# Kernel optimization log

Measured on AMD Instinct MI355X. Metric: run time of the kernel, lower is better.

## Reference

```python
import jax, jax.numpy as jnp
import numpy as np

N_HEADS = 16
LN_EPS = 1e-5


def setup_inputs() -> dict:
    key = jax.random.key(0)
    k_z, k_qkv, k_proj = jax.random.split(key, 3)
    b, n, dm = 4, 2048, 1024
    z = jax.random.normal(k_z, (b, n, dm), dtype=jnp.float32)
    gamma = jnp.ones((dm,), dtype=jnp.float32)
    beta = jnp.zeros((dm,), dtype=jnp.float32)
    # parameterize Linear weights as (in, out) so y = x @ w (same math as torch x @ W.T)
    w_qkv = jax.random.normal(k_qkv, (dm, 3 * dm), dtype=jnp.float32) * (1.0 / np.sqrt(dm))
    w_proj = jax.random.normal(k_proj, (dm, dm), dtype=jnp.float32) * (1.0 / np.sqrt(dm))
    b_proj = jnp.zeros((dm,), dtype=jnp.float32)
    return {"z": z, "gamma": gamma, "beta": beta, "w_qkv": w_qkv,
            "w_proj": w_proj, "b_proj": b_proj}


def reference(z, gamma, beta, w_qkv, w_proj, b_proj):
    b, n, dm = z.shape
    h = N_HEADS
    d = dm // h
    scaling = jnp.asarray(np.sqrt(dm / h), dtype=z.dtype)

    # LayerNorm over last dim
    mu = jnp.mean(z, axis=-1, keepdims=True)
    var = jnp.mean(jnp.square(z - mu), axis=-1, keepdims=True)
    zn = (z - mu) * jax.lax.rsqrt(var + LN_EPS) * gamma + beta

    qkv = zn @ w_qkv  # [b, n, 3*dm]
    # einops 'b n (h d qkv_n) -> qkv_n b h n d': qkv index is INNERMOST of packed dim
    qkv = qkv.reshape(b, n, h, d, 3)
    q = qkv[..., 0]  # [b, n, h, d]
    k = qkv[..., 1]
    v = qkv[..., 2]

    scores = jnp.einsum('bqhd,bkhd->bhqk', q, k) / scaling  # [b, h, n, n]
    att = jax.nn.softmax(scores, axis=-1)
    out = jnp.einsum('bhqk,bkhd->bqhd', att, v).reshape(b, n, dm)
    out = out @ w_proj + b_proj  # projection (drop_hidden=False); dropout is identity in eval
    return z + out
```

## Files before the change

kernel.cpp:

```cpp
#include <hip/hip_runtime.h>

typedef unsigned short ushort;
typedef unsigned int uint;

typedef __bf16 bf16x8 __attribute__((ext_vector_type(8)));
typedef float floatx4 __attribute__((ext_vector_type(4)));

constexpr int BATCH = 4;
constexpr int SEQ = 2048;
constexpr int DM = 1024;
constexpr int NH = 16;
constexpr int HD = 64;
constexpr int M = BATCH * SEQ;
constexpr int NQKV = 3 * DM;
constexpr float QSCALE = 0.18033688011112042f;

__device__ __forceinline__ ushort f2b(float f) {
    uint x; __builtin_memcpy(&x, &f, 4);
    x += 0x7fffu + ((x >> 16) & 1u);
    return (ushort)(x >> 16);
}

__device__ __forceinline__ void gload16(const ushort* g, ushort* l) {
    __builtin_amdgcn_global_load_lds(
        (const __attribute__((address_space(1))) void*)g,
        (__attribute__((address_space(3))) void*)l, 16, 0, 0);
}

__global__ __launch_bounds__(256) void prep_kernel(
    const float* __restrict__ w_qkv, ushort* __restrict__ wqT,
    const float* __restrict__ w_proj, ushort* __restrict__ wpT,
    const float* __restrict__ z, const float* __restrict__ gamma,
    const float* __restrict__ beta, ushort* __restrict__ zn) {
    __shared__ ushort tile[64][65];
    int id = blockIdx.x;
    int t = threadIdx.x;
    if (id < 1024) {
        int tx = t & 63, ty = t >> 6;
        if (id < 768) {
            int bx = id % 48, by = id / 48;
            int c0 = bx * 64, r0 = by * 64;
#pragma unroll
            for (int i = 0; i < 64; i += 4)
                tile[i + ty][tx] = f2b(w_qkv[(size_t)(r0 + i + ty) * NQKV + c0 + tx]);
            __syncthreads();
#pragma unroll
            for (int i = 0; i < 64; i += 4) {
                int c = c0 + i + ty;
                int cp = (c % 3) * DM + c / 3;
                wqT[(size_t)cp * DM + r0 + tx] = tile[tx][i + ty];
            }
        } else {
            int q = id - 768;
            int c0 = (q % 16) * 64, r0 = (q / 16) * 64;
#pragma unroll
            for (int i = 0; i < 64; i += 4)
                tile[i + ty][tx] = f2b(w_proj[(size_t)(r0 + i + ty) * DM + c0 + tx]);
            __syncthreads();
#pragma unroll
            for (int i = 0; i < 64; i += 4)
                wpT[(size_t)(c0 + i + ty) * DM + r0 + tx] = tile[tx][i + ty];
        }
        return;
    }
    int row = id - 1024;
    float4 v = reinterpret_cast<const float4*>(z + (size_t)row * DM)[t];
    float s = v.x + v.y + v.z + v.w;
    float sq = v.x * v.x + v.y * v.y + v.z * v.z + v.w * v.w;
#pragma unroll
    for (int off = 32; off >= 1; off >>= 1) {
        s  += __shfl_xor(s, off);
        sq += __shfl_xor(sq, off);
    }
    __shared__ float red[8];
    int wave = t >> 6;
    if ((t & 63) == 0) { red[wave] = s; red[wave + 4] = sq; }
    __syncthreads();
    s  = red[0] + red[1] + red[2] + red[3];
    sq = red[4] + red[5] + red[6] + red[7];
    float mean = s * (1.f / DM);
    float var  = sq * (1.f / DM) - mean * mean;
    float rstd = rsqrtf(var + 1e-5f);
    float4 g = reinterpret_cast<const float4*>(gamma)[t];
    float4 bt = reinterpret_cast<const float4*>(beta)[t];
    ushort4 o;
    o.x = f2b((v.x - mean) * rstd * g.x + bt.x);
    o.y = f2b((v.y - mean) * rstd * g.y + bt.y);
    o.z = f2b((v.z - mean) * rstd * g.z + bt.z);
    o.w = f2b((v.w - mean) * rstd * g.w + bt.w);
    reinterpret_cast<ushort4*>(zn + (size_t)row * DM)[t] = o;
}

__device__ __forceinline__ void gemm128_core(
    const ushort* __restrict__ A, const ushort* __restrict__ BT,
    int m0, int n0, int t, floatx4 (&acc)[4][4],
    ushort (*As)[64], ushort (*Bs)[64]) {
    int lane = t & 63, w = t >> 6;
    int l16 = lane & 15, quad = lane >> 4;
    int wm = (w >> 1) * 64, wn = (w & 1) * 64;
#pragma unroll
    for (int i = 0; i < 4; i++)
#pragma unroll
        for (int j = 0; j < 4; j++) acc[i][j] = (floatx4){0.f, 0.f, 0.f, 0.f};

    int srow8 = lane >> 3;
    int lseg = (lane & 7) ^ srow8;
    const ushort* gA[4]; const ushort* gB[4];
    ushort* lA[4]; ushort* lB[4];
#pragma unroll
    for (int c = 0; c < 4; c++) {
        int r = 32 * c + 8 * w + srow8;
        gA[c] = &A [(size_t)(m0 + r) * DM + lseg * 8];
        gB[c] = &BT[(size_t)(n0 + r) * DM + lseg * 8];
        lA[c] = &As[32 * c + 8 * w][0];
        lB[c] = &Bs[32 * c + 8 * w][0];
    }
    int sw = l16 & 7;

    for (int k0 = 0; k0 < DM; k0 += 64) {
#pragma unroll
        for (int c = 0; c < 4; c++) {
            gload16(gA[c] + k0, lA[c]);
            gload16(gB[c] + k0, lB[c]);
        }
        __syncthreads();
#pragma unroll
        for (int kk = 0; kk < 2; kk++) {
            bf16x8 af[4], bf[4];
#pragma unroll
            for (int i = 0; i < 4; i++)
                af[i] = *reinterpret_cast<const bf16x8*>(
                    &As[wm + i * 16 + l16][((kk * 4 + quad) ^ sw) << 3]);
#pragma unroll
            for (int j = 0; j < 4; j++)
                bf[j] = *reinterpret_cast<const bf16x8*>(
                    &Bs[wn + j * 16 + l16][((kk * 4 + quad) ^ sw) << 3]);
#pragma unroll
            for (int i = 0; i < 4; i++)
#pragma unroll
                for (int j = 0; j < 4; j++)
                    acc[i][j] = __builtin_amdgcn_mfma_f32_16x16x32_bf16(
                        af[i], bf[j], acc[i][j], 0, 0, 0);
        }
        __syncthreads();
    }
}

__global__ __launch_bounds__(256) void gemm_qkv(
    const ushort* __restrict__ A,
    const ushort* __restrict__ BT,
    ushort* __restrict__ Q, ushort* __restrict__ K, ushort* __restrict__ V) {
    __shared__ ushort smem[16384];
    ushort (*As)[64] = (ushort(*)[64])smem;
    ushort (*Bs)[64] = (ushort(*)[64])(smem + 8192);
    ushort* Cs = smem;
    int t = threadIdx.x;
    int id = blockIdx.x;
    int m0 = (id & 63) * 128, n0 = (id >> 6) * 128;
    floatx4 acc[4][4];
    gemm128_core(A, BT, m0, n0, t, acc, As, Bs);
    int lane = t & 63, w = t >> 6;
    int l16 = lane & 15, quad = lane >> 4;
    int wn = (w & 1) * 64;
    int which = n0 >> 10;
    int hd0 = n0 & 1023;
    float scale = (which == 0) ? QSCALE : 1.0f;
    int bb = m0 >> 11;
    int nb = m0 & 2047;
    ushort* dstQK = (which == 0) ? Q : K;

#pragma unroll
    for (int p = 0; p < 2; p++) {
        __syncthreads();
        if ((w >> 1) == p) {
            if (which < 2) {
#pragma unroll
                for (int i = 0; i < 4; i++)
#pragma unroll
                    for (int j = 0; j < 4; j++)
#pragma unroll
                        for (int r = 0; r < 4; r++)
                            Cs[(i * 16 + quad * 4 + r) * 136 + wn + j * 16 + l16] =
                                f2b(acc[i][j][r] * scale);
            } else {
#pragma unroll
                for (int i = 0; i < 4; i++)
#pragma unroll
                    for (int j = 0; j < 4; j++)
#pragma unroll
                        for (int r = 0; r < 4; r++)
                            Cs[(wn + j * 16 + l16) * 72 + i * 16 + quad * 4 + r] =
                                f2b(acc[i][j][r]);
            }
        }
        __syncthreads();
        if (which < 2) {
            int ch = (t & 15) * 8;
#pragma unroll
            for (int u = 0; u < 4; u++) {
                int lr = (t >> 4) + u * 16;
                int n = nb + p * 64 + lr;
                int hh = (hd0 + ch) >> 6, dd = ch & 63;
                *reinterpret_cast<uint4*>(
                    &dstQK[((size_t)((bb * NH + hh) * SEQ) + n) * HD + dd]) =
                    *reinterpret_cast<const uint4*>(&Cs[lr * 136 + ch]);
            }
        } else {
            int nch = (t & 7) * 8;
#pragma unroll
            for (int u = 0; u < 4; u++) {
                int dc = (t >> 3) + u * 32;
                int hh = (hd0 >> 6) + (dc >> 6), dd = dc & 63;
                int n = nb + p * 64 + nch;
                *reinterpret_cast<uint4*>(
                    &V[((size_t)((bb * NH + hh) * HD) + dd) * SEQ + n]) =
                    *reinterpret_cast<const uint4*>(&Cs[dc * 72 + nch]);
            }
        }
    }
}

__global__ __launch_bounds__(256) void gemm_proj(
    const ushort* __restrict__ A,
    const ushort* __restrict__ BT,
    const float* __restrict__ bias, const float* __restrict__ z,
    float* __restrict__ out) {
    __shared__ ushort As[128][64];
    __shared__ ushort Bs[128][64];
    int t = threadIdx.x;
    int id = blockIdx.x;
    int m0 = (id & 63) * 128, n0 = (id >> 6) * 128;
    floatx4 acc[4][4];
    gemm128_core(A, BT, m0, n0, t, acc, As, Bs);
    int lane = t & 63, w = t >> 6;
    int l16 = lane & 15, quad = lane >> 4;
    int wm = (w >> 1) * 64, wn = (w & 1) * 64;
#pragma unroll
    for (int j = 0; j < 4; j++) {
        int col = n0 + wn + j * 16 + l16;
        float bz = bias[col];
#pragma unroll
        for (int i = 0; i < 4; i++) {
#pragma unroll
            for (int r = 0; r < 4; r++) {
                int row = m0 + wm + i * 16 + quad * 4 + r;
                out[(size_t)row * DM + col] =
                    acc[i][j][r] + bz + z[(size_t)row * DM + col];
            }
        }
    }
}

__global__ __launch_bounds__(256) void attn_kernel(
    const ushort* __restrict__ Q, const ushort* __restrict__ K,
    const ushort* __restrict__ Vt, ushort* __restrict__ O) {
    __shared__ ushort QsPs[128 * 64];
    __shared__ ushort Ks[64 * 64];
    __shared__ ushort Vs[64 * 64];
    int t = threadIdx.x;
    int lane = t & 63, w = t >> 6;
    int l16 = lane & 15, quad = lane >> 4;
    int id = blockIdx.x;
    int qt = id >> 6, bh = id & 63;
    int bb = bh >> 4, h = bh & 15;
    int q0 = qt * 128;
    const ushort* Qg = Q  + (size_t)((bb * NH + h) * SEQ + q0) * HD;
    const ushort* Kg = K  + (size_t)((bb * NH + h) * SEQ) * HD;
    const ushort* Vg = Vt + (size_t)((bb * NH + h) * HD) * SEQ;

    int srow = lane >> 3;
    int lseg = (lane & 7) ^ srow;
    int r0 = 8 * w + srow;

    gload16(Qg + (size_t)r0 * HD + lseg * 8,         &QsPs[w * 512]);
    gload16(Qg + (size_t)(32 + r0) * HD + lseg * 8,  &QsPs[2048 + w * 512]);
    gload16(Qg + (size_t)(64 + r0) * HD + lseg * 8,  &QsPs[4096 + w * 512]);
    gload16(Qg + (size_t)(96 + r0) * HD + lseg * 8,  &QsPs[6144 + w * 512]);
    gload16(Kg + (size_t)r0 * HD + lseg * 8,         &Ks[w * 512]);
    gload16(Kg + (size_t)(32 + r0) * HD + lseg * 8,  &Ks[2048 + w * 512]);
    gload16(Vg + (size_t)r0 * SEQ + lseg * 8,        &Vs[w * 512]);
    gload16(Vg + (size_t)(32 + r0) * SEQ + lseg * 8, &Vs[2048 + w * 512]);
    __syncthreads();

    int swl = l16 & 7;
    bf16x8 aq[2][2];
    ushort* PsRow[2];
#pragma unroll
    for (int g = 0; g < 2; g++) {
        int row = 32 * w + 16 * g + l16;
        aq[g][0] = *reinterpret_cast<const bf16x8*>(&QsPs[row * 64 + ((quad ^ swl) << 3)]);
        aq[g][1] = *reinterpret_cast<const bf16x8*>(&QsPs[row * 64 + (((quad + 4) ^ swl) << 3)]);
        PsRow[g] = &QsPs[row * 64];
    }

    size_t koff1 = (size_t)r0 * HD + lseg * 8;
    size_t koff2 = (size_t)(32 + r0) * HD + lseg * 8;
    size_t voff1 = (size_t)r0 * SEQ + lseg * 8;
    size_t voff2 = (size_t)(32 + r0) * SEQ + lseg * 8;
    ushort* kw1 = &Ks[w * 512 + (lane & 63) * 8];
    ushort* kw2 = &Ks[2048 + w * 512 + (lane & 63) * 8];
    ushort* vw1 = &Vs[w * 512 + (lane & 63) * 8];
    ushort* vw2 = &Vs[2048 + w * 512 + (lane & 63) * 8];
    const ushort* Kp = Kg + (size_t)64 * HD;
    const ushort* Vp = Vg + 64;

    bf16x8 bones;
    {
        union { ushort u[8]; bf16x8 v; } cvt;
        ushort one = (l16 == 0) ? (ushort)0x3F80 : (ushort)0;
#pragma unroll
        for (int i = 0; i < 8; i++) cvt.u[i] = one;
        bones = cvt.v;
    }

    floatx4 Oacc[2][4], lacc[2];
#pragma unroll
    for (int g = 0; g < 2; g++) {
        lacc[g] = (floatx4){0.f, 0.f, 0.f, 0.f};
#pragma unroll
        for (int tt = 0; tt < 4; tt++) Oacc[g][tt] = (floatx4){0.f, 0.f, 0.f, 0.f};
    }

    constexpr int NT = SEQ / 64;
    for (int kt = 0; kt < NT; kt++) {
        uint4 kr1 = *reinterpret_cast<const uint4*>(Kp + koff1);
        uint4 kr2 = *reinterpret_cast<const uint4*>(Kp + koff2);
        uint4 vr1 = *reinterpret_cast<const uint4*>(Vp + voff1);
        uint4 vr2 = *reinterpret_cast<const uint4*>(Vp + voff2);
        Kp += (size_t)64 * HD;
        Vp += 64;

        floatx4 sacc[2][4];
#pragma unroll
        for (int nt = 0; nt < 4; nt++) {
            bf16x8 ak0 = *reinterpret_cast<const bf16x8*>(&Ks[(nt * 16 + l16) * 64 + ((quad ^ swl) << 3)]);
            bf16x8 ak1 = *reinterpret_cast<const bf16x8*>(&Ks[(nt * 16 + l16) * 64 + (((quad + 4) ^ swl) << 3)]);
#pragma unroll
            for (int g = 0; g < 2; g++) {
                floatx4 sv = (floatx4){0.f, 0.f, 0.f, 0.f};
                sv = __builtin_amdgcn_mfma_f32_16x16x32_bf16(ak0, aq[g][0], sv, 0, 0, 0);
                sv = __builtin_amdgcn_mfma_f32_16x16x32_bf16(ak1, aq[g][1], sv, 0, 0, 0);
                sacc[g][nt] = sv;
            }
        }
#pragma unroll
        for (int g = 0; g < 2; g++) {
#pragma unroll
            for (int nt = 0; nt < 4; nt++) {
                float p0 = __builtin_amdgcn_exp2f(sacc[g][nt][0]);
                float p1 = __builtin_amdgcn_exp2f(sacc[g][nt][1]);
                float p2 = __builtin_amdgcn_exp2f(sacc[g][nt][2]);
                float p3 = __builtin_amdgcn_exp2f(sacc[g][nt][3]);
                uint b0, b1, b2, b3;
                __builtin_memcpy(&b0, &p0, 4); __builtin_memcpy(&b1, &p1, 4);
                __builtin_memcpy(&b2, &p2, 4); __builtin_memcpy(&b3, &p3, 4);
                uint2 pk;
                pk.x = __builtin_amdgcn_perm(b1, b0, 0x07060302u);
                pk.y = __builtin_amdgcn_perm(b3, b2, 0x07060302u);
                int lseg2 = 2 * nt + (quad >> 1);
                *reinterpret_cast<uint2*>(&PsRow[g][((lseg2 ^ swl) << 3) + (quad & 1) * 4]) = pk;
            }
        }
#pragma unroll
        for (int ks = 0; ks < 2; ks++) {
            bf16x8 ap[2];
#pragma unroll
            for (int g = 0; g < 2; g++) {
                ap[g] = *reinterpret_cast<const bf16x8*>(
                    &PsRow[g][(((4 * ks + quad) ^ swl) << 3)]);
                lacc[g] = __builtin_amdgcn_mfma_f32_16x16x32_bf16(ap[g], bones, lacc[g], 0, 0, 0);
            }
#pragma unroll
            for (int tt = 0; tt < 4; tt++) {
                bf16x8 bv = *reinterpret_cast<const bf16x8*>(
                    &Vs[(tt * 16 + l16) * 64 + ((((ks * 4 + quad)) ^ swl) << 3)]);
#pragma unroll
                for (int g = 0; g < 2; g++)
                    Oacc[g][tt] = __builtin_amdgcn_mfma_f32_16x16x32_bf16(ap[g], bv, Oacc[g][tt], 0, 0, 0);
            }
        }
        __syncthreads();
        *reinterpret_cast<uint4*>(kw1) = kr1;
        *reinterpret_cast<uint4*>(kw2) = kr2;
        *reinterpret_cast<uint4*>(vw1) = vr1;
        *reinterpret_cast<uint4*>(vw2) = vr2;
        __syncthreads();
    }
    float lq[2][4];
#pragma unroll
    for (int g = 0; g < 2; g++)
#pragma unroll
        for (int j = 0; j < 4; j++) lq[g][j] = __shfl(lacc[g][j], quad << 4);

#pragma unroll
    for (int g = 0; g < 2; g++) {
#pragma unroll
        for (int tt = 0; tt < 4; tt++) {
#pragma unroll
            for (int j = 0; j < 4; j++) {
                int n = q0 + 32 * w + 16 * g + quad * 4 + j;
                int dcol = tt * 16 + l16;
                float val = Oacc[g][tt][j] / lq[g][j];
                O[(size_t)(bb * SEQ + n) * DM + h * HD + dcol] = f2b(val);
            }
        }
    }
}

extern "C" void kernel_launch(void* const* d_in, const int* in_sizes, int n_in,
                              void* d_out, int out_size, void* d_ws, size_t ws_size,
                              hipStream_t stream) {
    const float* z      = (const float*)d_in[0];
    const float* gamma  = (const float*)d_in[1];
    const float* beta   = (const float*)d_in[2];
    const float* w_qkv  = (const float*)d_in[3];
    const float* w_proj = (const float*)d_in[4];
    const float* b_proj = (const float*)d_in[5];
    float* out = (float*)d_out;

    char* ws = (char*)d_ws;
    const size_t SZ = (size_t)M * DM * sizeof(ushort);
    ushort* zn   = (ushort*)(ws);
    ushort* Qb   = (ushort*)(ws + SZ);
    ushort* Kb   = (ushort*)(ws + 2 * SZ);
    ushort* Vb   = (ushort*)(ws + 3 * SZ);
    ushort* wqT  = (ushort*)(ws + 4 * SZ);
    ushort* wpT  = (ushort*)(ws + 4 * SZ + (size_t)DM * NQKV * sizeof(ushort));
    ushort* Ob = zn;

    prep_kernel<<<1024 + M, 256, 0, stream>>>(w_qkv, wqT, w_proj, wpT,
                                              z, gamma, beta, zn);
    gemm_qkv<<<(NQKV / 128) * 64, 256, 0, stream>>>(zn, wqT, Qb, Kb, Vb);
    attn_kernel<<<(SEQ / 128) * BATCH * NH, 256, 0, stream>>>(Qb, Kb, Vb, Ob);
    gemm_proj<<<(DM / 128) * 64, 256, 0, stream>>>(Ob, wpT, b_proj, z, out);
}
```

Measured before the change: 272.1 us.

## Double-buffer K tiles in LDS and cut one barrier per attention iteration

```diff
diff --git a/kernel.cpp b/kernel.cpp
--- a/kernel.cpp
+++ b/kernel.cpp
@@ -255,7 +255,7 @@
     const ushort* __restrict__ Q, const ushort* __restrict__ K,
     const ushort* __restrict__ Vt, ushort* __restrict__ O) {
     __shared__ ushort QsPs[128 * 64];
-    __shared__ ushort Ks[64 * 64];
+    __shared__ ushort Ks[2 * 64 * 64];
     __shared__ ushort Vs[64 * 64];
     int t = threadIdx.x;
     int lane = t & 63, w = t >> 6;
@@ -297,10 +297,10 @@
     size_t koff2 = (size_t)(32 + r0) * HD + lseg * 8;
     size_t voff1 = (size_t)r0 * SEQ + lseg * 8;
     size_t voff2 = (size_t)(32 + r0) * SEQ + lseg * 8;
-    ushort* kw1 = &Ks[w * 512 + (lane & 63) * 8];
-    ushort* kw2 = &Ks[2048 + w * 512 + (lane & 63) * 8];
-    ushort* vw1 = &Vs[w * 512 + (lane & 63) * 8];
-    ushort* vw2 = &Vs[2048 + w * 512 + (lane & 63) * 8];
+    int kwo1 = w * 512 + lane * 8;
+    int kwo2 = 2048 + w * 512 + lane * 8;
+    ushort* vw1 = &Vs[w * 512 + lane * 8];
+    ushort* vw2 = &Vs[2048 + w * 512 + lane * 8];
     const ushort* Kp = Kg + (size_t)64 * HD;
     const ushort* Vp = Vg + 64;
 
@@ -313,12 +313,13 @@
         bones = cvt.v;
     }
 
+    const floatx4 zero4 = (floatx4){0.f, 0.f, 0.f, 0.f};
     floatx4 Oacc[2][4], lacc[2];
 #pragma unroll
     for (int g = 0; g < 2; g++) {
-        lacc[g] = (floatx4){0.f, 0.f, 0.f, 0.f};
-#pragma unroll
-        for (int tt = 0; tt < 4; tt++) Oacc[g][tt] = (floatx4){0.f, 0.f, 0.f, 0.f};
+        lacc[g] = zero4;
+#pragma unroll
+        for (int tt = 0; tt < 4; tt++) Oacc[g][tt] = zero4;
     }
 
     constexpr int NT = SEQ / 64;
@@ -330,19 +331,24 @@
         Kp += (size_t)64 * HD;
         Vp += 64;
 
+        int cur = (kt & 1) << 12;
+        int nxt = cur ^ 4096;
+        const ushort* KsC = Ks + cur;
+
         floatx4 sacc[2][4];
+        __builtin_amdgcn_s_setprio(1);
 #pragma unroll
         for (int nt = 0; nt < 4; nt++) {
-            bf16x8 ak0 = *reinterpret_cast<const bf16x8*>(&Ks[(nt * 16 + l16) * 64 + ((quad ^ swl) << 3)]);
-            bf16x8 ak1 = *reinterpret_cast<const bf16x8*>(&Ks[(nt * 16 + l16) * 64 + (((quad + 4) ^ swl) << 3)]);
+            bf16x8 ak0 = *reinterpret_cast<const bf16x8*>(&KsC[(nt * 16 + l16) * 64 + ((quad ^ swl) << 3)]);
+            bf16x8 ak1 = *reinterpret_cast<const bf16x8*>(&KsC[(nt * 16 + l16) * 64 + (((quad + 4) ^ swl) << 3)]);
 #pragma unroll
             for (int g = 0; g < 2; g++) {
-                floatx4 sv = (floatx4){0.f, 0.f, 0.f, 0.f};
-                sv = __builtin_amdgcn_mfma_f32_16x16x32_bf16(ak0, aq[g][0], sv, 0, 0, 0);
+                floatx4 sv = __builtin_amdgcn_mfma_f32_16x16x32_bf16(ak0, aq[g][0], zero4, 0, 0, 0);
                 sv = __builtin_amdgcn_mfma_f32_16x16x32_bf16(ak1, aq[g][1], sv, 0, 0, 0);
                 sacc[g][nt] = sv;
             }
         }
+        __builtin_amdgcn_s_setprio(0);
 #pragma unroll
         for (int g = 0; g < 2; g++) {
 #pragma unroll
@@ -361,6 +367,12 @@
                 *reinterpret_cast<uint2*>(&PsRow[g][((lseg2 ^ swl) << 3) + (quad & 1) * 4]) = pk;
             }
         }
+        *reinterpret_cast<uint4*>(&Ks[nxt + kwo1]) = kr1;
+        *reinterpret_cast<uint4*>(&Ks[nxt + kwo2]) = kr2;
+
+        asm volatile("s_waitcnt lgkmcnt(0)\n\ts_barrier" ::: "memory");
+
+        __builtin_amdgcn_s_setprio(1);
 #pragma unroll
         for (int ks = 0; ks < 2; ks++) {
             bf16x8 ap[2];
@@ -379,12 +391,11 @@
                     Oacc[g][tt] = __builtin_amdgcn_mfma_f32_16x16x32_bf16(ap[g], bv, Oacc[g][tt], 0, 0, 0);
             }
         }
-        __syncthreads();
-        *reinterpret_cast<uint4*>(kw1) = kr1;
-        *reinterpret_cast<uint4*>(kw2) = kr2;
+        __builtin_amdgcn_s_setprio(0);
+
+        asm volatile("s_waitcnt lgkmcnt(0)\n\ts_barrier" ::: "memory");
         *reinterpret_cast<uint4*>(vw1) = vr1;
         *reinterpret_cast<uint4*>(vw2) = vr2;
-        __syncthreads();
     }
     float lq[2][4];
 #pragma unroll
```

Result: slower. 281.4 us (+3.4%).

## Rewrite QKV GEMM with 256x256 tiles, 512 threads and double-buffered LDS

Applied to the files above, without the earlier changes.

```diff
diff --git a/kernel.cpp b/kernel.cpp
--- a/kernel.cpp
+++ b/kernel.cpp
@@ -146,76 +146,144 @@
     }
 }
 
-__global__ __launch_bounds__(256) void gemm_qkv(
+__global__ __launch_bounds__(512) void gemm_qkv256(
     const ushort* __restrict__ A,
     const ushort* __restrict__ BT,
     ushort* __restrict__ Q, ushort* __restrict__ K, ushort* __restrict__ V) {
-    __shared__ ushort smem[16384];
-    ushort (*As)[64] = (ushort(*)[64])smem;
-    ushort (*Bs)[64] = (ushort(*)[64])(smem + 8192);
-    ushort* Cs = smem;
+    __shared__ ushort smem[65536];
     int t = threadIdx.x;
-    int id = blockIdx.x;
-    int m0 = (id & 63) * 128, n0 = (id >> 6) * 128;
-    floatx4 acc[4][4];
-    gemm128_core(A, BT, m0, n0, t, acc, As, Bs);
     int lane = t & 63, w = t >> 6;
     int l16 = lane & 15, quad = lane >> 4;
-    int wn = (w & 1) * 64;
+    int wm = w >> 2, wn = w & 3;
+    int id = blockIdx.x;
+    int m0 = (id & 31) * 256, n0 = (id >> 5) * 256;
+
+    int srow = t >> 3;
+    int sseg = (t & 7) ^ (srow & 7);
+    const ushort* gA[4]; const ushort* gB[4];
+#pragma unroll
+    for (int c = 0; c < 4; c++) {
+        int r = c * 64 + srow;
+        gA[c] = A  + (size_t)(m0 + r) * DM + sseg * 8;
+        gB[c] = BT + (size_t)(n0 + r) * DM + sseg * 8;
+    }
+    int wbase = w * 512;
+
+    auto stage = [&](int k0, int d) {
+        int ab = d * 16384, bb2 = 32768 + d * 16384;
+#pragma unroll
+        for (int c = 0; c < 4; c++) {
+            gload16(gA[c] + k0, &smem[ab  + c * 4096 + wbase]);
+            gload16(gB[c] + k0, &smem[bb2 + c * 4096 + wbase]);
+        }
+    };
+
+    floatx4 acc[8][4];
+#pragma unroll
+    for (int i = 0; i < 8; i++)
+#pragma unroll
+        for (int j = 0; j < 4; j++) acc[i][j] = (floatx4){0.f, 0.f, 0.f, 0.f};
+
+    int sw = l16 & 7;
+
+    stage(0, 0);
+    stage(64, 1);
+    for (int kt = 0; kt < 16; kt++) {
+        int d = kt & 1;
+        if (kt < 15)
+            asm volatile("s_waitcnt vmcnt(8)\n\ts_barrier" ::: "memory");
+        else
+            asm volatile("s_waitcnt vmcnt(0)\n\ts_barrier" ::: "memory");
+        int ab = d * 16384, bb2 = 32768 + d * 16384;
+#pragma unroll
+        for (int kk = 0; kk < 2; kk++) {
+            bf16x8 bf[4];
+#pragma unroll
+            for (int j = 0; j < 4; j++)
+                bf[j] = *reinterpret_cast<const bf16x8*>(
+                    &smem[bb2 + (wn * 64 + j * 16 + l16) * 64 +
+                          (((kk * 4 + quad) ^ sw) << 3)]);
+#pragma unroll
+            for (int ig = 0; ig < 2; ig++) {
+                bf16x8 af[4];
+#pragma unroll
+                for (int ii = 0; ii < 4; ii++)
+                    af[ii] = *reinterpret_cast<const bf16x8*>(
+                        &smem[ab + (wm * 128 + (ig * 4 + ii) * 16 + l16) * 64 +
+                              (((kk * 4 + quad) ^ sw) << 3)]);
+                __builtin_amdgcn_s_setprio(1);
+#pragma unroll
+                for (int ii = 0; ii < 4; ii++)
+#pragma unroll
+                    for (int j = 0; j < 4; j++)
+                        acc[ig * 4 + ii][j] = __builtin_amdgcn_mfma_f32_16x16x32_bf16(
+                            af[ii], bf[j], acc[ig * 4 + ii][j], 0, 0, 0);
+                __builtin_amdgcn_s_setprio(0);
+            }
+        }
+        asm volatile("s_waitcnt lgkmcnt(0)\n\ts_barrier" ::: "memory");
+        if (kt + 2 < 16) stage((kt + 2) * 64, d);
+    }
+
     int which = n0 >> 10;
     int hd0 = n0 & 1023;
+    int bbx = m0 >> 11;
+    int nb = m0 & 2047;
     float scale = (which == 0) ? QSCALE : 1.0f;
-    int bb = m0 >> 11;
-    int nb = m0 & 2047;
-    ushort* dstQK = (which == 0) ? Q : K;
-
-#pragma unroll
-    for (int p = 0; p < 2; p++) {
-        __syncthreads();
-        if ((w >> 1) == p) {
-            if (which < 2) {
-#pragma unroll
-                for (int i = 0; i < 4; i++)
+
+    if (which < 2) {
+        ushort* dst = (which == 0) ? Q : K;
+#pragma unroll
+        for (int p = 0; p < 2; p++) {
+            if (wm == p) {
+#pragma unroll
+                for (int i = 0; i < 8; i++)
 #pragma unroll
                     for (int j = 0; j < 4; j++)
 #pragma unroll
                         for (int r = 0; r < 4; r++)
-                            Cs[(i * 16 + quad * 4 + r) * 136 + wn + j * 16 + l16] =
+                            smem[(i * 16 + quad * 4 + r) * 264 + wn * 64 + j * 16 + l16] =
                                 f2b(acc[i][j][r] * scale);
-            } else {
-#pragma unroll
-                for (int i = 0; i < 4; i++)
+            }
+            asm volatile("s_waitcnt lgkmcnt(0)\n\ts_barrier" ::: "memory");
+            int ch = (t & 31) * 8;
+#pragma unroll
+            for (int u = 0; u < 8; u++) {
+                int r = (t >> 5) + u * 16;
+                int n = nb + p * 128 + r;
+                int col = hd0 + ch;
+                int hh = col >> 6, dd = col & 63;
+                *reinterpret_cast<uint4*>(
+                    &dst[((size_t)((bbx * NH + hh) * SEQ) + n) * HD + dd]) =
+                    *reinterpret_cast<const uint4*>(&smem[r * 264 + ch]);
+            }
+            asm volatile("s_waitcnt lgkmcnt(0)\n\ts_barrier" ::: "memory");
+        }
+    } else {
+#pragma unroll
+        for (int p = 0; p < 2; p++) {
+            if (wm == p) {
+#pragma unroll
+                for (int i = 0; i < 8; i++)
 #pragma unroll
                     for (int j = 0; j < 4; j++)
 #pragma unroll
                         for (int r = 0; r < 4; r++)
-                            Cs[(wn + j * 16 + l16) * 72 + i * 16 + quad * 4 + r] =
+                            smem[(wn * 64 + j * 16 + l16) * 136 + i * 16 + quad * 4 + r] =
                                 f2b(acc[i][j][r]);
             }
-        }
-        __syncthreads();
-        if (which < 2) {
-            int ch = (t & 15) * 8;
-#pragma unroll
-            for (int u = 0; u < 4; u++) {
-                int lr = (t >> 4) + u * 16;
-                int n = nb + p * 64 + lr;
-                int hh = (hd0 + ch) >> 6, dd = ch & 63;
+            asm volatile("s_waitcnt lgkmcnt(0)\n\ts_barrier" ::: "memory");
+            int nch = (t & 15) * 8;
+#pragma unroll
+            for (int u = 0; u < 8; u++) {
+                int dc = (t >> 4) + u * 32;
+                int hh = (hd0 >> 6) + (dc >> 6), dd = dc & 63;
+                int n = nb + p * 128 + nch;
                 *reinterpret_cast<uint4*>(
-                    &dstQK[((size_t)((bb * NH + hh) * SEQ) + n) * HD + dd]) =
-                    *reinterpret_cast<const uint4*>(&Cs[lr * 136 + ch]);
-            }
-        } else {
-            int nch = (t & 7) * 8;
-#pragma unroll
-            for (int u = 0; u < 4; u++) {
-                int dc = (t >> 3) + u * 32;
-                int hh = (hd0 >> 6) + (dc >> 6), dd = dc & 63;
-                int n = nb + p * 64 + nch;
-                *reinterpret_cast<uint4*>(
-                    &V[((size_t)((bb * NH + hh) * HD) + dd) * SEQ + n]) =
-                    *reinterpret_cast<const uint4*>(&Cs[dc * 72 + nch]);
-            }
+                    &V[((size_t)((bbx * NH + hh) * HD) + dd) * SEQ + n]) =
+                    *reinterpret_cast<const uint4*>(&smem[dc * 136 + nch]);
+            }
+            asm volatile("s_waitcnt lgkmcnt(0)\n\ts_barrier" ::: "memory");
         }
     }
 }
@@ -430,7 +498,7 @@
 
     prep_kernel<<<1024 + M, 256, 0, stream>>>(w_qkv, wqT, w_proj, wpT,
                                               z, gamma, beta, zn);
-    gemm_qkv<<<(NQKV / 128) * 64, 256, 0, stream>>>(zn, wqT, Qb, Kb, Vb);
+    gemm_qkv256<<<(M / 256) * (NQKV / 256), 512, 0, stream>>>(zn, wqT, Qb, Kb, Vb);
     attn_kernel<<<(SEQ / 128) * BATCH * NH, 256, 0, stream>>>(Qb, Kb, Vb, Ob);
     gemm_proj<<<(DM / 128) * 64, 256, 0, stream>>>(Ob, wpT, b_proj, z, out);
 }
```

Result: no change. 276.4 us (+1.6%).

## Keep attention P in registers via permlane swaps and drop the Q/P shared buffer

Applied to the files above, without the earlier changes.

```diff
diff --git a/kernel.cpp b/kernel.cpp
--- a/kernel.cpp
+++ b/kernel.cpp
@@ -25,6 +25,13 @@
     __builtin_amdgcn_global_load_lds(
         (const __attribute__((address_space(1))) void*)g,
         (__attribute__((address_space(3))) void*)l, 16, 0, 0);
+}
+
+__device__ __forceinline__ void pl32(uint &a, uint &b) {
+    asm volatile("v_permlane32_swap_b32 %0, %1" : "+v"(a), "+v"(b));
+}
+__device__ __forceinline__ void pl16(uint &a, uint &b) {
+    asm volatile("v_permlane16_swap_b32 %0, %1" : "+v"(a), "+v"(b));
 }
 
 __global__ __launch_bounds__(256) void prep_kernel(
@@ -251,10 +258,9 @@
     }
 }
 
-__global__ __launch_bounds__(256) void attn_kernel(
+__global__ __launch_bounds__(256, 6) void attn_kernel(
     const ushort* __restrict__ Q, const ushort* __restrict__ K,
     const ushort* __restrict__ Vt, ushort* __restrict__ O) {
-    __shared__ ushort QsPs[128 * 64];
     __shared__ ushort Ks[64 * 64];
     __shared__ ushort Vs[64 * 64];
     int t = threadIdx.x;
@@ -272,35 +278,38 @@
     int lseg = (lane & 7) ^ srow;
     int r0 = 8 * w + srow;
 
-    gload16(Qg + (size_t)r0 * HD + lseg * 8,         &QsPs[w * 512]);
-    gload16(Qg + (size_t)(32 + r0) * HD + lseg * 8,  &QsPs[2048 + w * 512]);
-    gload16(Qg + (size_t)(64 + r0) * HD + lseg * 8,  &QsPs[4096 + w * 512]);
-    gload16(Qg + (size_t)(96 + r0) * HD + lseg * 8,  &QsPs[6144 + w * 512]);
+    gload16(Qg + (size_t)r0 * HD + lseg * 8,         &Ks[w * 512]);
+    gload16(Qg + (size_t)(32 + r0) * HD + lseg * 8,  &Ks[2048 + w * 512]);
+    gload16(Qg + (size_t)(64 + r0) * HD + lseg * 8,  &Vs[w * 512]);
+    gload16(Qg + (size_t)(96 + r0) * HD + lseg * 8,  &Vs[2048 + w * 512]);
+    __syncthreads();
+
+    int swl = l16 & 7;
+    bf16x8 aq[2][2];
+    {
+        const ushort* Qh = (w < 2) ? Ks : Vs;
+#pragma unroll
+        for (int g = 0; g < 2; g++) {
+            int qr = 32 * (w & 1) + 16 * g + l16;
+            aq[g][0] = *reinterpret_cast<const bf16x8*>(&Qh[qr * 64 + ((quad ^ swl) << 3)]);
+            aq[g][1] = *reinterpret_cast<const bf16x8*>(&Qh[qr * 64 + (((quad + 4) ^ swl) << 3)]);
+        }
+    }
+    __syncthreads();
     gload16(Kg + (size_t)r0 * HD + lseg * 8,         &Ks[w * 512]);
     gload16(Kg + (size_t)(32 + r0) * HD + lseg * 8,  &Ks[2048 + w * 512]);
     gload16(Vg + (size_t)r0 * SEQ + lseg * 8,        &Vs[w * 512]);
     gload16(Vg + (size_t)(32 + r0) * SEQ + lseg * 8, &Vs[2048 + w * 512]);
     __syncthreads();
 
-    int swl = l16 & 7;
-    bf16x8 aq[2][2];
-    ushort* PsRow[2];
-#pragma unroll
-    for (int g = 0; g < 2; g++) {
-        int row = 32 * w + 16 * g + l16;
-        aq[g][0] = *reinterpret_cast<const bf16x8*>(&QsPs[row * 64 + ((quad ^ swl) << 3)]);
-        aq[g][1] = *reinterpret_cast<const bf16x8*>(&QsPs[row * 64 + (((quad + 4) ^ swl) << 3)]);
-        PsRow[g] = &QsPs[row * 64];
-    }
-
     size_t koff1 = (size_t)r0 * HD + lseg * 8;
     size_t koff2 = (size_t)(32 + r0) * HD + lseg * 8;
     size_t voff1 = (size_t)r0 * SEQ + lseg * 8;
     size_t voff2 = (size_t)(32 + r0) * SEQ + lseg * 8;
-    ushort* kw1 = &Ks[w * 512 + (lane & 63) * 8];
-    ushort* kw2 = &Ks[2048 + w * 512 + (lane & 63) * 8];
-    ushort* vw1 = &Vs[w * 512 + (lane & 63) * 8];
-    ushort* vw2 = &Vs[2048 + w * 512 + (lane & 63) * 8];
+    ushort* kw1 = &Ks[w * 512 + lane * 8];
+    ushort* kw2 = &Ks[2048 + w * 512 + lane * 8];
+    ushort* vw1 = &Vs[w * 512 + lane * 8];
+    ushort* vw2 = &Vs[2048 + w * 512 + lane * 8];
     const ushort* Kp = Kg + (size_t)64 * HD;
     const ushort* Vp = Vg + 64;
 
@@ -343,6 +352,7 @@
                 sacc[g][nt] = sv;
             }
         }
+        uint pkx[2][4], pky[2][4];
 #pragma unroll
         for (int g = 0; g < 2; g++) {
 #pragma unroll
@@ -354,11 +364,8 @@
                 uint b0, b1, b2, b3;
                 __builtin_memcpy(&b0, &p0, 4); __builtin_memcpy(&b1, &p1, 4);
                 __builtin_memcpy(&b2, &p2, 4); __builtin_memcpy(&b3, &p3, 4);
-                uint2 pk;
-                pk.x = __builtin_amdgcn_perm(b1, b0, 0x07060302u);
-                pk.y = __builtin_amdgcn_perm(b3, b2, 0x07060302u);
-                int lseg2 = 2 * nt + (quad >> 1);
-                *reinterpret_cast<uint2*>(&PsRow[g][((lseg2 ^ swl) << 3) + (quad & 1) * 4]) = pk;
+                pkx[g][nt] = __builtin_amdgcn_perm(b1, b0, 0x07060302u);
+                pky[g][nt] = __builtin_amdgcn_perm(b3, b2, 0x07060302u);
             }
         }
 #pragma unroll
@@ -366,8 +373,13 @@
             bf16x8 ap[2];
 #pragma unroll
             for (int g = 0; g < 2; g++) {
-                ap[g] = *reinterpret_cast<const bf16x8*>(
-                    &PsRow[g][(((4 * ks + quad) ^ swl) << 3)]);
+                uint a0 = pkx[g][2 * ks], b0 = pkx[g][2 * ks + 1];
+                uint a1 = pky[g][2 * ks], b1 = pky[g][2 * ks + 1];
+                pl32(a0, b0); pl32(a1, b1);
+                pl16(a0, b0); pl16(a1, b1);
+                union { uint u[4]; bf16x8 v; } cv;
+                cv.u[0] = a0; cv.u[1] = a1; cv.u[2] = b0; cv.u[3] = b1;
+                ap[g] = cv.v;
                 lacc[g] = __builtin_amdgcn_mfma_f32_16x16x32_bf16(ap[g], bones, lacc[g], 0, 0, 0);
             }
 #pragma unroll
```

Result: slower. 665.8 us (+144.7%).
